# Performance work log

Hardware: AMD Instinct MI355X
Metric: run time of the kernel (lower is better)

## Reference

```python
import jax, jax.numpy as jnp
import numpy as np

B, CIN, COUT, K, S, P, D = 4, 128, 128, 3, 1, 1, 1
H = W = 96
MASK_SCALE = 2.0


def setup_inputs() -> dict:
    key = jax.random.key(0)
    k1, k2, k3, k4 = jax.random.split(key, 4)
    x = jax.random.normal(k1, (B, CIN, H, W), jnp.float32)
    weight = jax.random.normal(k2, (COUT, CIN, K, K), jnp.float32) * 0.05
    bias = jax.random.normal(k3, (COUT,), jnp.float32) * 0.05
    # conv_offset_mask: out_channels = deformable_groups*3*K*K = 27, no bias
    w_offmask = jax.random.normal(k4, (3 * K * K, CIN, K, K), jnp.float32) * 0.01
    return {"x": x, "weight": weight, "bias": bias, "w_offmask": w_offmask}


def _bilinear_gather(x, py, px):
    """x: [B,C,H,W]; py,px: [B,K2,Ho,Wo] float sample coords.
    Returns [B,C,K2,Ho,Wo], zero outside image (per-corner validity as in DCNv2)."""
    Bn, C, Hh, Ww = x.shape
    K2, Ho, Wo = py.shape[1], py.shape[2], py.shape[3]
    y0 = jnp.floor(py); x0 = jnp.floor(px)
    ly = py - y0; lx = px - x0
    y0i = y0.astype(jnp.int32); x0i = x0.astype(jnp.int32)
    y1i = y0i + 1; x1i = x0i + 1
    x_flat = x.reshape(Bn, C, Hh * Ww)

    def corner(yi, xi, w):
        valid = (yi >= 0) & (yi < Hh) & (xi >= 0) & (xi < Ww)
        yc = jnp.clip(yi, 0, Hh - 1)
        xc = jnp.clip(xi, 0, Ww - 1)
        idx = (yc * Ww + xc).reshape(Bn, K2 * Ho * Wo)
        v = jnp.take_along_axis(x_flat, idx[:, None, :], axis=2)  # [B,C,K2*Ho*Wo]
        v = v.reshape(Bn, C, K2, Ho, Wo)
        wv = (w * valid.astype(x.dtype))[:, None]  # [B,1,K2,Ho,Wo]
        return v * wv

    out = corner(y0i, x0i, (1 - ly) * (1 - lx))
    out = out + corner(y0i, x1i, (1 - ly) * lx)
    out = out + corner(y1i, x0i, ly * (1 - lx))
    out = out + corner(y1i, x1i, ly * lx)
    return out


def reference(x, weight, bias, w_offmask):
    K2 = K * K
    # offset/mask conv (standard conv, no bias)
    om = jax.lax.conv_general_dilated(
        x, w_offmask, window_strides=(S, S), padding=[(P, P), (P, P)],
        dimension_numbers=("NCHW", "OIHW", "NCHW"))  # [B, 3*K2, Ho, Wo]
    o1 = om[:, :K2]
    o2 = om[:, K2:2 * K2]
    mask = jax.nn.sigmoid(om[:, 2 * K2:]) * MASK_SCALE  # [B,K2,Ho,Wo]
    offset = jnp.concatenate([o1, o2], axis=1)  # [B,2*K2,Ho,Wo]

    Ho, Wo = om.shape[2], om.shape[3]
    ki, kj = jnp.meshgrid(jnp.arange(K), jnp.arange(K), indexing="ij")
    ki = ki.reshape(K2); kj = kj.reshape(K2)
    ho = jnp.arange(Ho); wo = jnp.arange(Wo)
    base_y = (ho[None, :] * S - P + ki[:, None] * D).astype(x.dtype)  # [K2,Ho]
    base_x = (wo[None, :] * S - P + kj[:, None] * D).astype(x.dtype)  # [K2,Wo]
    py = base_y[None, :, :, None] + o1  # [B,K2,Ho,Wo]
    px = base_x[None, :, None, :] + o2

    sampled = _bilinear_gather(x, py, px)            # [B,C,K2,Ho,Wo]
    sampled = sampled * mask[:, None]                # modulation
    wr = weight.reshape(COUT, CIN, K2)
    out = jnp.einsum("ock,bckhw->bohw", wr, sampled) + bias[None, :, None, None]
    return out, offset
```

## Files before the change

kernel.cpp:

```cpp
#include <hip/hip_runtime.h>
#include <math.h>

#define HH 96
#define WW 96
#define HW (96*96)
#define CIN_ 128
#define COUT_ 128
#define OUT_ELEMS (4*128*96*96)
#define TPX 16

#define XT_OFF   0u
#define WBF_OFF  9437184u
#define WOMB_OFF 9732096u

typedef __attribute__((ext_vector_type(8))) short short8v;
typedef __attribute__((ext_vector_type(4))) float float4v;

__device__ __forceinline__ unsigned short f2bf(float f) {
    unsigned u = __builtin_bit_cast(unsigned, f);
    u += 0x7FFFu + ((u >> 16) & 1u);
    return (unsigned short)(u >> 16);
}
__device__ __forceinline__ unsigned rneu(float f) {
    unsigned u = __builtin_bit_cast(unsigned, f);
    return u + 0x7FFFu + ((u >> 16) & 1u);
}
__device__ __forceinline__ unsigned pkbf(float hi, float lo) {
    return __builtin_amdgcn_perm(rneu(hi), rneu(lo), 0x07060302u);
}
__device__ __forceinline__ float bflo(unsigned u) {
    return __builtin_bit_cast(float, u << 16);
}
__device__ __forceinline__ float bfhi(unsigned u) {
    return __builtin_bit_cast(float, u & 0xffff0000u);
}

#define BLOCK_SYNC() do {                                   \
    __builtin_amdgcn_sched_barrier(0);                      \
    asm volatile("s_waitcnt lgkmcnt(0)" ::: "memory");      \
    __builtin_amdgcn_s_barrier();                           \
    __builtin_amdgcn_sched_barrier(0);                      \
} while (0)

__global__ __launch_bounds__(256) void pre_kernel(
    const float* __restrict__ x, const float* __restrict__ w,
    const float* __restrict__ wom, unsigned short* __restrict__ xt,
    unsigned short* __restrict__ wbf, unsigned short* __restrict__ womb)
{
    __shared__ float tile[64][130];
    const int t = threadIdx.x;
    const int f = blockIdx.x;

    if (f < 576) {
        const int g  = (f & 7) * 72 + (f >> 3);
        const int b  = g / 144;
        const int p0 = (g - b * 144) * 64;
#pragma unroll
        for (int j = 0; j < 8; j++) {
            const int i  = j * 256 + t;
            const int c  = i >> 4;
            const int p4 = (i & 15) * 4;
            const float4 v = *(const float4*)(x + ((size_t)(b * CIN_ + c) * HW + p0 + p4));
            tile[p4 + 0][c] = v.x; tile[p4 + 1][c] = v.y;
            tile[p4 + 2][c] = v.z; tile[p4 + 3][c] = v.w;
        }
        __syncthreads();
#pragma unroll
        for (int j = 0; j < 8; j++) {
            const int i   = j * 256 + t;
            const int pxl = i >> 5;
            const int c4  = (i & 31) * 4;
            uint2 v;
            v.x = pkbf(tile[pxl][c4 + 1], tile[pxl][c4 + 0]);
            v.y = pkbf(tile[pxl][c4 + 3], tile[pxl][c4 + 2]);
            *(uint2*)(xt + ((size_t)(b * HW + p0 + pxl) * CIN_ + c4)) = v;
        }
    } else {
        const int i = (f - 576) * 256 + t;
        if (i < 147456) {
            const int frag = i >> 9;
            const int lane = (i >> 3) & 63;
            const int e    = i & 7;
            const int mt = frag / 36, r = frag - mt * 36;
            const int kc = r >> 2, kst = r & 3;
            const int m = lane & 15, quad = lane >> 4;
            const int oc = mt * 16 + m;
            const int c  = kst * 32 + quad * 8 + e;
            wbf[i] = f2bf(w[(size_t)oc * 1152 + c * 9 + kc]);
        } else {
            const int i2 = i - 147456;
            const int frag = i2 >> 9;
            const int lane = (i2 >> 3) & 63;
            const int e    = i2 & 7;
            const int mt = frag / 36, r = frag - mt * 36;
            const int kc = r >> 2, kst = r & 3;
            const int m = lane & 15, quad = lane >> 4;
            const int row = mt * 16 + m;
            const int c   = kst * 32 + quad * 8 + e;
            womb[i2] = (row < 27) ? f2bf(wom[(size_t)row * 1152 + c * 9 + kc]) : 0;
        }
    }
}

__global__ __launch_bounds__(128, 4) void dconv_small(
    const unsigned short* __restrict__ xt, const unsigned short* __restrict__ wbf,
    const unsigned short* __restrict__ womb, const float* __restrict__ bias,
    float* __restrict__ out, float* __restrict__ off_out)
{
    __shared__ int smem[3632];
    int*   btile0 = smem;
    int*   btile1 = smem + 1024;
    int*   sprep  = smem + 2048;
    float* som    = (float*)(smem + 3200);

    const int t    = threadIdx.x;
    const int wave = __builtin_amdgcn_readfirstlane(t >> 6);
    const int lane = t & 63;
    const int quad = lane >> 4;
    const int m    = lane & 15;
    const int l32  = lane & 31;
    const int half = lane >> 5;

    const int f  = blockIdx.x;
    const int c2 = (f & 7) * 288 + (f >> 3);
    const int b  = c2 / 576;
    const int p0 = (c2 - b * 576) * TPX;

    const unsigned short* xtb = xt + (size_t)b * HW * CIN_;
    const char* xtB = (const char*)xtb;

    const int h  = p0 / 96;
    const int w0 = p0 - h * 96;

#pragma unroll
    for (int k = 0; k < 7; k++) {
        const int i = k * 128 + t;
        if (i < 864) {
            const int row = i >> 4;
            const int ch  = i & 15;
            const int r   = row / 18;
            const int cc  = row - r * 18;
            const int y   = h + r - 1;
            const int xx  = w0 + cc - 1;
            uint4 v = make_uint4(0u, 0u, 0u, 0u);
            if (((unsigned)y < 96u) && ((unsigned)xx < 96u))
                v = *(const uint4*)(xtb + (size_t)(y * 96 + xx) * CIN_ + ch * 8);
            *(uint4*)&smem[row * 64 + ((ch ^ (row & 7)) << 2)] = v;
        }
    }
    __syncthreads();

    float4v acc2;
#pragma unroll
    for (int r = 0; r < 4; r++) acc2[r] = 0.f;
    {
        const short* wfB = (const short*)womb + (size_t)wave * 36 * 512 + lane * 8;
#pragma unroll
        for (int kc = 0; kc < 9; kc++) {
            const int ki = kc / 3, kj = kc - 3 * (kc / 3);
            const int sr = ki * 18 + m + kj;
            const short* brow = (const short*)smem + sr * 128;
#pragma unroll
            for (int kst = 0; kst < 4; kst++) {
                const int c16s = (kst * 4 + quad) ^ (sr & 7);
                const short8v bfv = *(const short8v*)(brow + c16s * 8);
                const short8v av  = *(const short8v*)(wfB + (kc * 4 + kst) * 512);
                acc2 = __builtin_amdgcn_mfma_f32_16x16x32_bf16(av, bfv, acc2, 0, 0, 0);
            }
        }
    }
    __syncthreads();

    {
#pragma unroll
        for (int r = 0; r < 4; r++) {
            const int oc = wave * 16 + quad * 4 + r;
            if (oc < 27) som[oc * 16 + m] = acc2[r];
            if (oc < 18) off_out[(size_t)(b * 18 + oc) * HW + p0 + m] = acc2[r];
        }
    }
    __syncthreads();

#pragma unroll
    for (int k = 0; k < 2; k++) {
        const int it = k * 128 + t;
        if (it < 144) {
            const int kc = it >> 4;
            const int px = it & 15;
            const int ki = kc / 3, kj = kc - 3 * (kc / 3);

            const float o1 = som[kc * 16 + px];
            const float o2 = som[(9 + kc) * 16 + px];
            const float mr = som[(18 + kc) * 16 + px];
            const float mk = 2.f / (1.f + __expf(-mr));

            const float py  = (float)(h - 1 + ki) + o1;
            const float pxf = (float)(w0 + px - 1 + kj) + o2;
            const float y0f = floorf(py), x0f = floorf(pxf);
            const float ly = py - y0f,    lx = pxf - x0f;
            const int y0 = (int)y0f, x0 = (int)x0f;
            const int y1 = y0 + 1,   x1 = x0 + 1;

            const float w00 = (1.f - ly) * (1.f - lx), w01 = (1.f - ly) * lx;
            const float w10 = ly * (1.f - lx),         w11 = ly * lx;

            const int yc0 = min(max(y0, 0), HH - 1), yc1 = min(max(y1, 0), HH - 1);
            const int xc0 = min(max(x0, 0), WW - 1), xc1 = min(max(x1, 0), WW - 1);
            const bool vy0 = (y0 >= 0) && (y0 < HH), vy1 = (y1 >= 0) && (y1 < HH);
            const bool vx0 = (x0 >= 0) && (x0 < WW), vx1 = (x1 >= 0) && (x1 < WW);

            sprep[it * 8 + 0] = yc0 * 96 + xc0;
            sprep[it * 8 + 1] = yc0 * 96 + xc1;
            sprep[it * 8 + 2] = yc1 * 96 + xc0;
            sprep[it * 8 + 3] = yc1 * 96 + xc1;
            sprep[it * 8 + 4] = __builtin_bit_cast(int, (vy0 && vx0) ? mk * w00 : 0.f);
            sprep[it * 8 + 5] = __builtin_bit_cast(int, (vy0 && vx1) ? mk * w01 : 0.f);
            sprep[it * 8 + 6] = __builtin_bit_cast(int, (vy1 && vx0) ? mk * w10 : 0.f);
            sprep[it * 8 + 7] = __builtin_bit_cast(int, (vy1 && vx1) ? mk * w11 : 0.f);
        }
    }
    __syncthreads();

    uint2 gbuf[4][4];

#define ISSUE(SL, KCV, ITV) do {                                              \
    const int pxl_ = wave * 8 + (ITV) * 2 + half;                             \
    const int4 id4_ = *(const int4*)&sprep[((KCV) * 16 + pxl_) * 8];          \
    const unsigned co_ = (unsigned)l32 << 3;                                  \
    gbuf[SL][0] = *(const uint2*)(xtB + (((unsigned)id4_.x << 8) | co_));     \
    gbuf[SL][1] = *(const uint2*)(xtB + (((unsigned)id4_.y << 8) | co_));     \
    gbuf[SL][2] = *(const uint2*)(xtB + (((unsigned)id4_.z << 8) | co_));     \
    gbuf[SL][3] = *(const uint2*)(xtB + (((unsigned)id4_.w << 8) | co_));     \
} while (0)

#define COMBINE(SL, IV) do {                                                  \
    const int pxl_ = wave * 8 + (IV) * 2 + half;                              \
    const float4 w4_ = *(const float4*)&sprep[(kc * 16 + pxl_) * 8 + 4];      \
    const uint2 u0 = gbuf[SL][0], u1 = gbuf[SL][1];                           \
    const uint2 u2 = gbuf[SL][2], u3 = gbuf[SL][3];                           \
    const float v0 = w4_.x*bflo(u0.x) + w4_.y*bflo(u1.x) + w4_.z*bflo(u2.x) + w4_.w*bflo(u3.x); \
    const float v1 = w4_.x*bfhi(u0.x) + w4_.y*bfhi(u1.x) + w4_.z*bfhi(u2.x) + w4_.w*bfhi(u3.x); \
    const float v2 = w4_.x*bflo(u0.y) + w4_.y*bflo(u1.y) + w4_.z*bflo(u2.y) + w4_.w*bflo(u3.y); \
    const float v3 = w4_.x*bfhi(u0.y) + w4_.y*bfhi(u1.y) + w4_.z*bfhi(u2.y) + w4_.w*bfhi(u3.y); \
    uint2 o_;                                                                 \
    o_.x = pkbf(v1, v0);                                                      \
    o_.y = pkbf(v3, v2);                                                      \
    *(uint2*)&bt[pxl_ * 64 + (((l32 >> 1) ^ (pxl_ & 7)) << 2) + ((l32 & 1) << 1)] = o_; \
} while (0)

    float4v acc[4];
#pragma unroll
    for (int j = 0; j < 4; j++)
#pragma unroll
        for (int r = 0; r < 4; r++) acc[j][r] = 0.f;

    const char* wfrag = (const char*)wbf + ((size_t)wave * 4 * 36) * 1024 + lane * 16;

    ISSUE(0, 0, 0);
    ISSUE(1, 0, 1);
    ISSUE(2, 0, 2);
    ISSUE(3, 0, 3);

    for (int kc = 0; kc < 9; kc++) {
        int* bt = (kc & 1) ? btile1 : btile0;

        COMBINE(0, 0);
        if (kc < 8) ISSUE(0, kc + 1, 0);
        COMBINE(1, 1);
        if (kc < 8) ISSUE(1, kc + 1, 1);
        COMBINE(2, 2);
        if (kc < 8) ISSUE(2, kc + 1, 2);
        COMBINE(3, 3);
        if (kc < 8) ISSUE(3, kc + 1, 3);

        BLOCK_SYNC();

#pragma unroll
        for (int kst = 0; kst < 4; kst++) {
            const short8v bfv = *(const short8v*)((const short*)bt
                + 2 * (m * 64 + (((kst * 4 + quad) ^ (m & 7)) << 2)));
#pragma unroll
            for (int mt = 0; mt < 4; mt++) {
                const short8v af = *(const short8v*)(wfrag
                    + ((size_t)(mt * 36 + kc * 4 + kst)) * 1024);
                acc[mt] = __builtin_amdgcn_mfma_f32_16x16x32_bf16(af, bfv, acc[mt], 0, 0, 0);
            }
        }
    }
#undef ISSUE
#undef COMBINE

#pragma unroll
    for (int mt = 0; mt < 4; mt++) {
#pragma unroll
        for (int r = 0; r < 4; r++) {
            const int oc = wave * 64 + mt * 16 + quad * 4 + r;
            out[(size_t)(b * COUT_ + oc) * HW + p0 + m] = acc[mt][r] + bias[oc];
        }
    }
}

extern "C" void kernel_launch(void* const* d_in, const int* in_sizes, int n_in,
                              void* d_out, int out_size, void* d_ws, size_t ws_size,
                              hipStream_t stream) {
    const float* x      = (const float*)d_in[0];
    const float* weight = (const float*)d_in[1];
    const float* bias   = (const float*)d_in[2];
    const float* wom    = (const float*)d_in[3];

    float* out     = (float*)d_out;
    float* off_out = out + OUT_ELEMS;

    unsigned short* xtb  = (unsigned short*)((char*)d_ws + XT_OFF);
    unsigned short* wbf  = (unsigned short*)((char*)d_ws + WBF_OFF);
    unsigned short* womb = (unsigned short*)((char*)d_ws + WOMB_OFF);

    pre_kernel <<<dim3(1296), 256, 0, stream>>>(x, weight, wom, xtb, wbf, womb);
    dconv_small<<<dim3(2304), 128, 0, stream>>>(xtb, wbf, womb, bias, out, off_out);
}
```

Before: 131.9 us.

## Load halo tile via global_load_lds, relayout weight fragments, split offset-conv accumulators

```diff
diff --git a/kernel.cpp b/kernel.cpp
--- a/kernel.cpp
+++ b/kernel.cpp
@@ -78,14 +78,15 @@
     } else {
         const int i = (f - 576) * 256 + t;
         if (i < 147456) {
-            const int frag = i >> 9;
+            const int F    = i >> 9;
             const int lane = (i >> 3) & 63;
             const int e    = i & 7;
-            const int mt = frag / 36, r = frag - mt * 36;
-            const int kc = r >> 2, kst = r & 3;
-            const int m = lane & 15, quad = lane >> 4;
-            const int oc = mt * 16 + m;
-            const int c  = kst * 32 + quad * 8 + e;
+            const int kc  = F >> 5;
+            const int r   = F & 31;
+            const int kst = r >> 3;
+            const int mt8 = r & 7;
+            const int oc  = mt8 * 16 + (lane & 15);
+            const int c   = kst * 32 + (lane >> 4) * 8 + e;
             wbf[i] = f2bf(w[(size_t)oc * 1152 + c * 9 + kc]);
         } else {
             const int i2 = i - 147456;
@@ -94,9 +95,8 @@
             const int e    = i2 & 7;
             const int mt = frag / 36, r = frag - mt * 36;
             const int kc = r >> 2, kst = r & 3;
-            const int m = lane & 15, quad = lane >> 4;
-            const int row = mt * 16 + m;
-            const int c   = kst * 32 + quad * 8 + e;
+            const int row = mt * 16 + (lane & 15);
+            const int c   = kst * 32 + (lane >> 4) * 8 + e;
             womb[i2] = (row < 27) ? f2bf(wom[(size_t)row * 1152 + c * 9 + kc]) : 0;
         }
     }
@@ -137,22 +137,31 @@
         const int i = k * 128 + t;
         if (i < 864) {
             const int row = i >> 4;
-            const int ch  = i & 15;
+            const int lin = i & 15;
             const int r   = row / 18;
             const int cc  = row - r * 18;
             const int y   = h + r - 1;
             const int xx  = w0 + cc - 1;
-            uint4 v = make_uint4(0u, 0u, 0u, 0u);
-            if (((unsigned)y < 96u) && ((unsigned)xx < 96u))
-                v = *(const uint4*)(xtb + (size_t)(y * 96 + xx) * CIN_ + ch * 8);
-            *(uint4*)&smem[row * 64 + ((ch ^ (row & 7)) << 2)] = v;
+            if (((unsigned)y < 96u) && ((unsigned)xx < 96u)) {
+                const unsigned short* gsrc = xtb
+                    + (size_t)(y * 96 + xx) * CIN_ + (lin ^ (row & 7)) * 8;
+                __builtin_amdgcn_global_load_lds(
+                    (const __attribute__((address_space(1))) unsigned int*)gsrc,
+                    (__attribute__((address_space(3))) unsigned int*)
+                        (smem + (k * 128 + wave * 64) * 4),
+                    16, 0, 0);
+            } else {
+                *(int4*)&smem[i * 4] = make_int4(0, 0, 0, 0);
+            }
         }
     }
     __syncthreads();
 
-    float4v acc2;
-#pragma unroll
-    for (int r = 0; r < 4; r++) acc2[r] = 0.f;
+    float4v acg[4];
+#pragma unroll
+    for (int j = 0; j < 4; j++)
+#pragma unroll
+        for (int r = 0; r < 4; r++) acg[j][r] = 0.f;
     {
         const short* wfB = (const short*)womb + (size_t)wave * 36 * 512 + lane * 8;
 #pragma unroll
@@ -165,7 +174,7 @@
                 const int c16s = (kst * 4 + quad) ^ (sr & 7);
                 const short8v bfv = *(const short8v*)(brow + c16s * 8);
                 const short8v av  = *(const short8v*)(wfB + (kc * 4 + kst) * 512);
-                acc2 = __builtin_amdgcn_mfma_f32_16x16x32_bf16(av, bfv, acc2, 0, 0, 0);
+                acg[kst] = __builtin_amdgcn_mfma_f32_16x16x32_bf16(av, bfv, acg[kst], 0, 0, 0);
             }
         }
     }
@@ -174,9 +183,10 @@
     {
 #pragma unroll
         for (int r = 0; r < 4; r++) {
+            const float v = (acg[0][r] + acg[1][r]) + (acg[2][r] + acg[3][r]);
             const int oc = wave * 16 + quad * 4 + r;
-            if (oc < 27) som[oc * 16 + m] = acc2[r];
-            if (oc < 18) off_out[(size_t)(b * 18 + oc) * HW + p0 + m] = acc2[r];
+            if (oc < 27) som[oc * 16 + m] = v;
+            if (oc < 18) off_out[(size_t)(b * 18 + oc) * HW + p0 + m] = v;
         }
     }
     __syncthreads();
@@ -209,10 +219,10 @@
             const bool vy0 = (y0 >= 0) && (y0 < HH), vy1 = (y1 >= 0) && (y1 < HH);
             const bool vx0 = (x0 >= 0) && (x0 < WW), vx1 = (x1 >= 0) && (x1 < WW);
 
-            sprep[it * 8 + 0] = yc0 * 96 + xc0;
-            sprep[it * 8 + 1] = yc0 * 96 + xc1;
-            sprep[it * 8 + 2] = yc1 * 96 + xc0;
-            sprep[it * 8 + 3] = yc1 * 96 + xc1;
+            sprep[it * 8 + 0] = (yc0 * 96 + xc0) << 8;
+            sprep[it * 8 + 1] = (yc0 * 96 + xc1) << 8;
+            sprep[it * 8 + 2] = (yc1 * 96 + xc0) << 8;
+            sprep[it * 8 + 3] = (yc1 * 96 + xc1) << 8;
             sprep[it * 8 + 4] = __builtin_bit_cast(int, (vy0 && vx0) ? mk * w00 : 0.f);
             sprep[it * 8 + 5] = __builtin_bit_cast(int, (vy0 && vx1) ? mk * w01 : 0.f);
             sprep[it * 8 + 6] = __builtin_bit_cast(int, (vy1 && vx0) ? mk * w10 : 0.f);
@@ -222,15 +232,15 @@
     __syncthreads();
 
     uint2 gbuf[4][4];
+    const unsigned co_ = (unsigned)l32 << 3;
 
 #define ISSUE(SL, KCV, ITV) do {                                              \
     const int pxl_ = wave * 8 + (ITV) * 2 + half;                             \
     const int4 id4_ = *(const int4*)&sprep[((KCV) * 16 + pxl_) * 8];          \
-    const unsigned co_ = (unsigned)l32 << 3;                                  \
-    gbuf[SL][0] = *(const uint2*)(xtB + (((unsigned)id4_.x << 8) | co_));     \
-    gbuf[SL][1] = *(const uint2*)(xtB + (((unsigned)id4_.y << 8) | co_));     \
-    gbuf[SL][2] = *(const uint2*)(xtB + (((unsigned)id4_.z << 8) | co_));     \
-    gbuf[SL][3] = *(const uint2*)(xtB + (((unsigned)id4_.w << 8) | co_));     \
+    gbuf[SL][0] = *(const uint2*)(xtB + ((unsigned)id4_.x | co_));            \
+    gbuf[SL][1] = *(const uint2*)(xtB + ((unsigned)id4_.y | co_));            \
+    gbuf[SL][2] = *(const uint2*)(xtB + ((unsigned)id4_.z | co_));            \
+    gbuf[SL][3] = *(const uint2*)(xtB + ((unsigned)id4_.w | co_));            \
 } while (0)
 
 #define COMBINE(SL, IV) do {                                                  \
@@ -254,7 +264,7 @@
 #pragma unroll
         for (int r = 0; r < 4; r++) acc[j][r] = 0.f;
 
-    const char* wfrag = (const char*)wbf + ((size_t)wave * 4 * 36) * 1024 + lane * 16;
+    const char* aw = (const char*)wbf + ((size_t)wave << 12) + lane * 16;
 
     ISSUE(0, 0, 0);
     ISSUE(1, 0, 1);
@@ -275,14 +285,15 @@
 
         BLOCK_SYNC();
 
+        const char* ak = aw + kc * 32768;
 #pragma unroll
         for (int kst = 0; kst < 4; kst++) {
             const short8v bfv = *(const short8v*)((const short*)bt
                 + 2 * (m * 64 + (((kst * 4 + quad) ^ (m & 7)) << 2)));
+            const char* aks = ak + kst * 8192;
 #pragma unroll
             for (int mt = 0; mt < 4; mt++) {
-                const short8v af = *(const short8v*)(wfrag
-                    + ((size_t)(mt * 36 + kc * 4 + kst)) * 1024);
+                const short8v af = *(const short8v*)(aks + mt * 1024);
                 acc[mt] = __builtin_amdgcn_mfma_f32_16x16x32_bf16(af, bfv, acc[mt], 0, 0, 0);
             }
         }
```

Result: slower. 140.9 us (+6.8%).
